# Performance work log

Hardware: AMD Instinct MI355X
Metric: run time of the kernel (lower is better)

The kernel has to match this reference:

```python
import jax, jax.numpy as jnp
import numpy as np


def setup_inputs() -> dict:
    key = jax.random.key(0)
    k1, k2, k3, k4 = jax.random.split(key, 4)
    B, C, H, W = 8, 256, 64, 64
    x = jax.random.normal(k1, (B, C, H, W), dtype=jnp.float32)
    wq = jax.random.normal(k2, (1, C), dtype=jnp.float32) * (1.0 / np.sqrt(C))
    wk = jax.random.normal(k3, (1, C), dtype=jnp.float32) * (1.0 / np.sqrt(C))
    wv = jax.random.normal(k4, (C, C), dtype=jnp.float32) * (1.0 / np.sqrt(C))
    gamma = jnp.zeros((1,), dtype=jnp.float32)
    return {"x": x, "wq": wq, "wk": wk, "wv": wv, "gamma": gamma}


def reference(x, wq, wk, wv, gamma):
    B, C, H, W = x.shape
    N = H * W
    xf = x.reshape(B, C, N)                      # [B, C, N]
    # 1x1 convs == channel matmuls
    f = jnp.einsum('oc,bcn->bon', wq, xf)        # [B, 1, N]
    g = jnp.einsum('oc,bcn->bon', wk, xf)        # [B, 1, N]
    h = jnp.einsum('oc,bcn->bon', wv, xf)        # [B, C, N]
    # scores[b, i, j] = f[b, 0, i] * g[b, 0, j]  -> [B, N, N]
    scores = jnp.einsum('bi,bj->bij', f[:, 0, :], g[:, 0, :])
    # softmax over dim=1 (rows), matching torch F.softmax(..., dim=1)
    beta = jax.nn.softmax(scores, axis=1)        # [B, N, N]
    gam = gamma[0]
    o = (1.0 - gam) * jnp.einsum('bcn,bnm->bcm', h, beta) + gam * xf
    return o.reshape(B, C, H, W)
```

## Files before the change

kernel.cpp:

```cpp
#include <hip/hip_runtime.h>
#include <math.h>

#define BQ 8
#define CQ 256
#define NQ 4096
#define MT 128
#define NSTEP (NQ / 32)

typedef short s16x8 __attribute__((ext_vector_type(8)));
typedef short s16x4 __attribute__((ext_vector_type(4)));
typedef float f32x4 __attribute__((ext_vector_type(4)));

static __device__ __forceinline__ float4 ld4(const float* p) { return *(const float4*)p; }

static constexpr float LOG2E = 1.4426950408889634f;

static __device__ __forceinline__ short f2bf(float f) {
    return __builtin_bit_cast(short, (__bf16)f);
}

__global__ void k_fg(const float* __restrict__ x, const float* __restrict__ wq,
                     const float* __restrict__ wk, float* __restrict__ fs,
                     float* __restrict__ g, short* __restrict__ xbf) {
    int b = blockIdx.y;
    int nloc = threadIdx.x & 63;
    int cg = threadIdx.x >> 6;
    int n = blockIdx.x * 64 + nloc;
    const float* xb = x + (size_t)b * CQ * NQ + n;
    short* xo = xbf + (size_t)b * CQ * NQ + n;
    float accf = 0.f, accg = 0.f;
    int c0 = cg * 64;
#pragma unroll 8
    for (int c = c0; c < c0 + 64; ++c) {
        float v = xb[(size_t)c * NQ];
        accf = fmaf(wq[c], v, accf);
        accg = fmaf(wk[c], v, accg);
        xo[(size_t)c * NQ] = f2bf(v);
    }
    __shared__ float sf[4][64], sg2[4][64];
    sf[cg][nloc] = accf;
    sg2[cg][nloc] = accg;
    __syncthreads();
    if (threadIdx.x < 64) {
        float f = sf[0][nloc] + sf[1][nloc] + sf[2][nloc] + sf[3][nloc];
        float gg = sg2[0][nloc] + sg2[1][nloc] + sg2[2][nloc] + sg2[3][nloc];
        fs[b * NQ + blockIdx.x * 64 + nloc] = f * LOG2E;
        g[b * NQ + blockIdx.x * 64 + nloc] = gg;
    }
}

__global__ void k_minmax(const float* __restrict__ fs, float* __restrict__ fmx,
                         float* __restrict__ fmn) {
    int b = blockIdx.x;
    const float* f = fs + b * NQ;
    float mx = -1e30f, mn = 1e30f;
    for (int i = threadIdx.x; i < NQ; i += 256) {
        float v = f[i];
        mx = fmaxf(mx, v);
        mn = fminf(mn, v);
    }
    for (int off = 32; off; off >>= 1) {
        mx = fmaxf(mx, __shfl_down(mx, off));
        mn = fminf(mn, __shfl_down(mn, off));
    }
    __shared__ float smx[4], smn[4];
    int wid = threadIdx.x >> 6;
    if ((threadIdx.x & 63) == 0) { smx[wid] = mx; smn[wid] = mn; }
    __syncthreads();
    if (threadIdx.x == 0) {
        mx = fmaxf(fmaxf(smx[0], smx[1]), fmaxf(smx[2], smx[3]));
        mn = fminf(fminf(smn[0], smn[1]), fminf(smn[2], smn[3]));
        fmx[b] = mx;
        fmn[b] = mn;
    }
}

__global__ void __launch_bounds__(256, 2) k_attn(
    const short* __restrict__ xbf, const float* __restrict__ fsp,
    const float* __restrict__ gp, const float* __restrict__ fmxs,
    const float* __restrict__ fmns, const float* __restrict__ wv,
    const float* __restrict__ x, const float* __restrict__ gamma,
    float* __restrict__ out) {
    __shared__ __align__(16) char smem[65536];

    int bid = blockIdx.x;
    int b = bid & 7;
    int mblk = bid >> 3;
    int m0 = mblk * MT;
    int tid = threadIdx.x;
    int l = tid & 63;
    int w = tid >> 6;
    int wc = w & 1;
    int wm = w >> 1;
    int q = l >> 4;
    int cr = l & 15;

    float fmx = fmxs[b], fmn = fmns[b];
    const float* gb = gp + b * NQ;
    float gj[4], nM[4], zac[4];
#pragma unroll
    for (int jm = 0; jm < 4; ++jm) {
        float gv = gb[m0 + wm * 64 + jm * 16 + cr];
        gj[jm] = gv;
        nM[jm] = -((gv >= 0.f) ? gv * fmx : gv * fmn);
        zac[jm] = 0.f;
    }

    const float* fb = fsp + b * NQ;
    const short* xb = xbf + (size_t)b * CQ * NQ;

    f32x4 acc[8][4];
#pragma unroll
    for (int jc = 0; jc < 8; ++jc)
#pragma unroll
        for (int jm = 0; jm < 4; ++jm) acc[jc][jm] = (f32x4){0.f, 0.f, 0.f, 0.f};

#pragma unroll
    for (int r2 = 0; r2 < 4; ++r2) {
        int off = tid * 16 + r2 * 4096;
        int row = off >> 6, nb = off & 63;
        const short* src = xb + (size_t)row * NQ + (nb >> 1);
        __builtin_amdgcn_global_load_lds(
            (const __attribute__((address_space(1))) void*)src,
            (__attribute__((address_space(3))) void*)(smem + off), 16, 0, 0);
    }
    float4 fqa = *(const float4*)(fb + q * 8);
    float4 fqb = *(const float4*)(fb + q * 8 + 4);
    __syncthreads();

    for (int t = 0; t < NSTEP; ++t) {
        const char* cbuf = smem + (t & 1) * 16384;
        int n0n = ((t + 1) & (NSTEP - 1)) * 32;
        if (t + 1 < NSTEP) {
            char* nbuf = smem + ((t + 1) & 1) * 16384;
#pragma unroll
            for (int r2 = 0; r2 < 4; ++r2) {
                int off = tid * 16 + r2 * 4096;
                int row = off >> 6, nb = off & 63;
                const short* src = xb + (size_t)row * NQ + n0n + (nb >> 1);
                __builtin_amdgcn_global_load_lds(
                    (const __attribute__((address_space(1))) void*)src,
                    (__attribute__((address_space(3))) void*)(nbuf + off), 16, 0, 0);
            }
        }
        float4 fqa_n = *(const float4*)(fb + n0n + q * 8);
        float4 fqb_n = *(const float4*)(fb + n0n + q * 8 + 4);
        float fq[8] = {fqa.x, fqa.y, fqa.z, fqa.w, fqb.x, fqb.y, fqb.z, fqb.w};
        s16x8 bv[4];
#pragma unroll
        for (int jm = 0; jm < 4; ++jm) {
            float z = zac[jm];
#pragma unroll
            for (int i = 0; i < 8; ++i) {
                float e = __builtin_amdgcn_exp2f(fmaf(fq[i], gj[jm], nM[jm]));
                z += e;
                bv[jm][i] = f2bf(e);
            }
            zac[jm] = z;
        }
#pragma unroll
        for (int jc = 0; jc < 8; ++jc) {
            s16x8 av = *(const s16x8*)(cbuf + (wc * 128 + jc * 16 + cr) * 64 + q * 16);
#pragma unroll
            for (int jm = 0; jm < 4; ++jm)
                acc[jc][jm] = __builtin_amdgcn_mfma_f32_16x16x32_bf16(av, bv[jm], acc[jc][jm], 0, 0, 0);
        }
        fqa = fqa_n;
        fqb = fqb_n;
        __syncthreads();
    }

    float rzl[4];
#pragma unroll
    for (int jm = 0; jm < 4; ++jm) {
        float z = zac[jm];
        z += __shfl_xor(z, 16);
        z += __shfl_xor(z, 32);
        rzl[jm] = 1.0f / z;
    }

#pragma unroll
    for (int jc = 0; jc < 8; ++jc) {
#pragma unroll
        for (int jm = 0; jm < 4; ++jm) {
            int mloc = wm * 64 + jm * 16 + cr;
            int cb = (wc * 256 + jc * 32 + q * 8) ^ ((mloc & 7) << 4);
            s16x4 v;
#pragma unroll
            for (int r = 0; r < 4; ++r) v[r] = f2bf(acc[jc][jm][r] * rzl[jm]);
            *(s16x4*)(smem + mloc * 512 + cb) = v;
        }
    }
    __syncthreads();

    int co0 = w * 64;
    f32x4 acc2[4][8];
#pragma unroll
    for (int j2 = 0; j2 < 4; ++j2)
#pragma unroll
        for (int jm2 = 0; jm2 < 8; ++jm2) acc2[j2][jm2] = (f32x4){0.f, 0.f, 0.f, 0.f};

#pragma unroll 2
    for (int ks = 0; ks < 8; ++ks) {
        s16x8 a2[4];
#pragma unroll
        for (int j2 = 0; j2 < 4; ++j2) {
            const float* wr = wv + (size_t)(co0 + j2 * 16 + cr) * CQ + ks * 32 + q * 8;
            float4 wa = ld4(wr);
            float4 wb = ld4(wr + 4);
            a2[j2][0] = f2bf(wa.x); a2[j2][1] = f2bf(wa.y);
            a2[j2][2] = f2bf(wa.z); a2[j2][3] = f2bf(wa.w);
            a2[j2][4] = f2bf(wb.x); a2[j2][5] = f2bf(wb.y);
            a2[j2][6] = f2bf(wb.z); a2[j2][7] = f2bf(wb.w);
        }
#pragma unroll
        for (int jm2 = 0; jm2 < 8; ++jm2) {
            int mloc = jm2 * 16 + cr;
            s16x8 b2 = *(const s16x8*)(smem + mloc * 512 + ((ks * 64 + q * 16) ^ ((mloc & 7) << 4)));
#pragma unroll
            for (int j2 = 0; j2 < 4; ++j2)
                acc2[j2][jm2] = __builtin_amdgcn_mfma_f32_16x16x32_bf16(a2[j2], b2, acc2[j2][jm2], 0, 0, 0);
        }
    }

    float gam = gamma[0];
    float omg = 1.f - gam;
    if (gam != 0.f) {
#pragma unroll
        for (int j2 = 0; j2 < 4; ++j2)
#pragma unroll
            for (int jm2 = 0; jm2 < 8; ++jm2)
#pragma unroll
                for (int r = 0; r < 4; ++r) {
                    int c_out = co0 + j2 * 16 + q * 4 + r;
                    size_t idx = ((size_t)b * CQ + c_out) * NQ + m0 + jm2 * 16 + cr;
                    __builtin_nontemporal_store(
                        fmaf(gam, x[idx], acc2[j2][jm2][r] * omg), out + idx);
                }
    } else {
#pragma unroll
        for (int j2 = 0; j2 < 4; ++j2)
#pragma unroll
            for (int jm2 = 0; jm2 < 8; ++jm2)
#pragma unroll
                for (int r = 0; r < 4; ++r) {
                    int c_out = co0 + j2 * 16 + q * 4 + r;
                    size_t idx = ((size_t)b * CQ + c_out) * NQ + m0 + jm2 * 16 + cr;
                    __builtin_nontemporal_store(acc2[j2][jm2][r] * omg, out + idx);
                }
    }
}

extern "C" void kernel_launch(void* const* d_in, const int* in_sizes, int n_in,
                              void* d_out, int out_size, void* d_ws, size_t ws_size,
                              hipStream_t stream) {
    const float* x     = (const float*)d_in[0];
    const float* wq    = (const float*)d_in[1];
    const float* wk    = (const float*)d_in[2];
    const float* wv    = (const float*)d_in[3];
    const float* gamma = (const float*)d_in[4];
    float* out = (float*)d_out;

    float* ws  = (float*)d_ws;
    float* fs  = ws;
    float* g   = ws + BQ * NQ;
    float* fmx = ws + 2 * BQ * NQ;
    float* fmn = fmx + BQ;
    short* xbf = (short*)(ws + 2 * BQ * NQ + 64);

    hipLaunchKernelGGL(k_fg, dim3(NQ / 64, BQ), dim3(256), 0, stream, x, wq, wk, fs, g, xbf);
    hipLaunchKernelGGL(k_minmax, dim3(BQ), dim3(256), 0, stream, fs, fmx, fmn);
    hipLaunchKernelGGL(k_attn, dim3(BQ * (NQ / MT)), dim3(256), 0, stream,
                       xbf, fs, g, fmx, fmn, wv, x, gamma, out);
}
```

Baseline: 135.8 us.

## Split attention K-loop across wave pairs with 4-stage LDS ring

Doubles the attention block to 512 threads. Wave pairs now alternate over the N reduction steps, with each pair's partial accumulators and softmax denominators merged through LDS. The x tile moves from double buffering to a 4-deep ring prefetched three steps ahead, and the f vector is staged once into LDS instead of being loaded from global memory every step. The aim is more waves per CU and better hiding of load latency in the exp+MFMA loop. The costs are a larger LDS footprint, an extra merge pass, and half of the waves sitting idle on alternate steps.

```diff
diff --git a/kernel.cpp b/kernel.cpp
--- a/kernel.cpp
+++ b/kernel.cpp
@@ -75,13 +75,18 @@
     }
 }
 
-__global__ void __launch_bounds__(256, 2) k_attn(
+#define RING_OFF 0
+#define FLDS_OFF 131072
+#define ZBUF_OFF 147456
+#define SMEM_BYTES 149504
+
+__global__ void __launch_bounds__(512, 2) k_attn(
     const short* __restrict__ xbf, const float* __restrict__ fsp,
     const float* __restrict__ gp, const float* __restrict__ fmxs,
     const float* __restrict__ fmns, const float* __restrict__ wv,
     const float* __restrict__ x, const float* __restrict__ gamma,
     float* __restrict__ out) {
-    __shared__ __align__(16) char smem[65536];
+    __shared__ __align__(16) char smem[SMEM_BYTES];
 
     int bid = blockIdx.x;
     int b = bid & 7;
@@ -90,10 +95,33 @@
     int tid = threadIdx.x;
     int l = tid & 63;
     int w = tid >> 6;
-    int wc = w & 1;
-    int wm = w >> 1;
+    int ws = w & 1;
+    int wm = (w >> 1) & 1;
+    int wc = w >> 2;
     int q = l >> 4;
     int cr = l & 15;
+
+    const short* xb = xbf + (size_t)b * CQ * NQ;
+    const float* fb = fsp + b * NQ;
+
+#pragma unroll
+    for (int r2 = 0; r2 < 2; ++r2) {
+        int off = tid * 16 + r2 * 8192;
+        __builtin_amdgcn_global_load_lds(
+            (const __attribute__((address_space(1))) void*)(fb + (off >> 2)),
+            (__attribute__((address_space(3))) void*)(smem + FLDS_OFF + off), 16, 0, 0);
+    }
+#pragma unroll
+    for (int c3 = 0; c3 < 3; ++c3) {
+#pragma unroll
+        for (int r2 = 0; r2 < 2; ++r2) {
+            int off = tid * 16 + r2 * 8192;
+            int row = off >> 6, nb = off & 63;
+            __builtin_amdgcn_global_load_lds(
+                (const __attribute__((address_space(1))) void*)(xb + (size_t)row * NQ + c3 * 32 + (nb >> 1)),
+                (__attribute__((address_space(3))) void*)(smem + c3 * 16384 + off), 16, 0, 0);
+        }
+    }
 
     float fmx = fmxs[b], fmn = fmns[b];
     const float* gb = gp + b * NQ;
@@ -106,105 +134,127 @@
         zac[jm] = 0.f;
     }
 
-    const float* fb = fsp + b * NQ;
-    const short* xb = xbf + (size_t)b * CQ * NQ;
-
     f32x4 acc[8][4];
 #pragma unroll
     for (int jc = 0; jc < 8; ++jc)
 #pragma unroll
         for (int jm = 0; jm < 4; ++jm) acc[jc][jm] = (f32x4){0.f, 0.f, 0.f, 0.f};
 
-#pragma unroll
-    for (int r2 = 0; r2 < 4; ++r2) {
-        int off = tid * 16 + r2 * 4096;
-        int row = off >> 6, nb = off & 63;
-        const short* src = xb + (size_t)row * NQ + (nb >> 1);
-        __builtin_amdgcn_global_load_lds(
-            (const __attribute__((address_space(1))) void*)src,
-            (__attribute__((address_space(3))) void*)(smem + off), 16, 0, 0);
-    }
-    float4 fqa = *(const float4*)(fb + q * 8);
-    float4 fqb = *(const float4*)(fb + q * 8 + 4);
-    __syncthreads();
-
     for (int t = 0; t < NSTEP; ++t) {
-        const char* cbuf = smem + (t & 1) * 16384;
-        int n0n = ((t + 1) & (NSTEP - 1)) * 32;
-        if (t + 1 < NSTEP) {
-            char* nbuf = smem + ((t + 1) & 1) * 16384;
-#pragma unroll
-            for (int r2 = 0; r2 < 4; ++r2) {
-                int off = tid * 16 + r2 * 4096;
+        asm volatile("s_waitcnt vmcnt(4)" ::: "memory");
+        __builtin_amdgcn_s_barrier();
+        {
+            int chunk = (t + 3) & (NSTEP - 1);
+            char* nbuf = smem + ((t + 3) & 3) * 16384;
+#pragma unroll
+            for (int r2 = 0; r2 < 2; ++r2) {
+                int off = tid * 16 + r2 * 8192;
                 int row = off >> 6, nb = off & 63;
-                const short* src = xb + (size_t)row * NQ + n0n + (nb >> 1);
                 __builtin_amdgcn_global_load_lds(
-                    (const __attribute__((address_space(1))) void*)src,
+                    (const __attribute__((address_space(1))) void*)(xb + (size_t)row * NQ + chunk * 32 + (nb >> 1)),
                     (__attribute__((address_space(3))) void*)(nbuf + off), 16, 0, 0);
             }
         }
-        float4 fqa_n = *(const float4*)(fb + n0n + q * 8);
-        float4 fqb_n = *(const float4*)(fb + n0n + q * 8 + 4);
-        float fq[8] = {fqa.x, fqa.y, fqa.z, fqa.w, fqb.x, fqb.y, fqb.z, fqb.w};
-        s16x8 bv[4];
-#pragma unroll
-        for (int jm = 0; jm < 4; ++jm) {
-            float z = zac[jm];
-#pragma unroll
-            for (int i = 0; i < 8; ++i) {
-                float e = __builtin_amdgcn_exp2f(fmaf(fq[i], gj[jm], nM[jm]));
-                z += e;
-                bv[jm][i] = f2bf(e);
+        if ((t & 1) == ws) {
+            const char* cbuf = smem + (t & 3) * 16384;
+            const float* fls = (const float*)(smem + FLDS_OFF) + t * 32;
+            float4 fqa = *(const float4*)(fls + q * 8);
+            float4 fqb = *(const float4*)(fls + q * 8 + 4);
+            float fq[8] = {fqa.x, fqa.y, fqa.z, fqa.w, fqb.x, fqb.y, fqb.z, fqb.w};
+            s16x8 bv[4];
+#pragma unroll
+            for (int jm = 0; jm < 4; ++jm) {
+                float z = zac[jm];
+#pragma unroll
+                for (int i = 0; i < 8; ++i) {
+                    float e = __builtin_amdgcn_exp2f(fmaf(fq[i], gj[jm], nM[jm]));
+                    z += e;
+                    bv[jm][i] = f2bf(e);
+                }
+                zac[jm] = z;
             }
-            zac[jm] = z;
-        }
-#pragma unroll
-        for (int jc = 0; jc < 8; ++jc) {
-            s16x8 av = *(const s16x8*)(cbuf + (wc * 128 + jc * 16 + cr) * 64 + q * 16);
-#pragma unroll
-            for (int jm = 0; jm < 4; ++jm)
-                acc[jc][jm] = __builtin_amdgcn_mfma_f32_16x16x32_bf16(av, bv[jm], acc[jc][jm], 0, 0, 0);
-        }
-        fqa = fqa_n;
-        fqb = fqb_n;
-        __syncthreads();
-    }
-
-    float rzl[4];
+#pragma unroll
+            for (int jc = 0; jc < 8; ++jc) {
+                s16x8 av = *(const s16x8*)(cbuf + (wc * 128 + jc * 16 + cr) * 64 + q * 16);
+#pragma unroll
+                for (int jm = 0; jm < 4; ++jm)
+                    acc[jc][jm] = __builtin_amdgcn_mfma_f32_16x16x32_bf16(av, bv[jm], acc[jc][jm], 0, 0, 0);
+            }
+        }
+    }
+    __syncthreads();
+
+    float zf[4];
 #pragma unroll
     for (int jm = 0; jm < 4; ++jm) {
         float z = zac[jm];
         z += __shfl_xor(z, 16);
         z += __shfl_xor(z, 32);
-        rzl[jm] = 1.0f / z;
-    }
-
-#pragma unroll
-    for (int jc = 0; jc < 8; ++jc) {
-#pragma unroll
-        for (int jm = 0; jm < 4; ++jm) {
-            int mloc = wm * 64 + jm * 16 + cr;
-            int cb = (wc * 256 + jc * 32 + q * 8) ^ ((mloc & 7) << 4);
-            s16x4 v;
-#pragma unroll
-            for (int r = 0; r < 4; ++r) v[r] = f2bf(acc[jc][jm][r] * rzl[jm]);
-            *(s16x4*)(smem + mloc * 512 + cb) = v;
-        }
-    }
-    __syncthreads();
-
-    int co0 = w * 64;
-    f32x4 acc2[4][8];
-#pragma unroll
-    for (int j2 = 0; j2 < 4; ++j2)
+        zf[jm] = z;
+    }
+    float* zb = (float*)(smem + ZBUF_OFF);
+    if (q == 0) {
+#pragma unroll
+        for (int jm = 0; jm < 4; ++jm) zb[w * 64 + jm * 16 + cr] = zf[jm];
+    }
+    __syncthreads();
+#pragma unroll
+    for (int jm = 0; jm < 4; ++jm) zf[jm] += zb[(w ^ 1) * 64 + jm * 16 + cr];
+
+    {
+        int p = wc * 2 + wm;
+        float* mrg = (float*)(smem + p * 32768);
+        if (ws == 1) {
+#pragma unroll
+            for (int jc = 0; jc < 8; ++jc)
+#pragma unroll
+                for (int jm = 0; jm < 4; ++jm)
+                    *(f32x4*)(mrg + ((jc * 4 + jm) * 64 + l) * 4) = acc[jc][jm];
+        }
+        __syncthreads();
+        if (ws == 0) {
+#pragma unroll
+            for (int jc = 0; jc < 8; ++jc)
+#pragma unroll
+                for (int jm = 0; jm < 4; ++jm) {
+                    f32x4 o = *(const f32x4*)(mrg + ((jc * 4 + jm) * 64 + l) * 4);
+                    acc[jc][jm] += o;
+                }
+        }
+        __syncthreads();
+    }
+
+    if (ws == 0) {
+        float rzl[4];
+#pragma unroll
+        for (int jm = 0; jm < 4; ++jm) rzl[jm] = 1.0f / zf[jm];
+#pragma unroll
+        for (int jc = 0; jc < 8; ++jc) {
+#pragma unroll
+            for (int jm = 0; jm < 4; ++jm) {
+                int mloc = wm * 64 + jm * 16 + cr;
+                int cb = (wc * 256 + jc * 32 + q * 8) ^ ((mloc & 7) << 4);
+                s16x4 v;
+#pragma unroll
+                for (int r = 0; r < 4; ++r) v[r] = f2bf(acc[jc][jm][r] * rzl[jm]);
+                *(s16x4*)(smem + mloc * 512 + cb) = v;
+            }
+        }
+    }
+    __syncthreads();
+
+    int co0 = w * 32;
+    f32x4 acc2[2][8];
+#pragma unroll
+    for (int j2 = 0; j2 < 2; ++j2)
 #pragma unroll
         for (int jm2 = 0; jm2 < 8; ++jm2) acc2[j2][jm2] = (f32x4){0.f, 0.f, 0.f, 0.f};
 
 #pragma unroll 2
     for (int ks = 0; ks < 8; ++ks) {
-        s16x8 a2[4];
-#pragma unroll
-        for (int j2 = 0; j2 < 4; ++j2) {
+        s16x8 a2[2];
+#pragma unroll
+        for (int j2 = 0; j2 < 2; ++j2) {
             const float* wr = wv + (size_t)(co0 + j2 * 16 + cr) * CQ + ks * 32 + q * 8;
             float4 wa = ld4(wr);
             float4 wb = ld4(wr + 4);
@@ -218,7 +268,7 @@
             int mloc = jm2 * 16 + cr;
             s16x8 b2 = *(const s16x8*)(smem + mloc * 512 + ((ks * 64 + q * 16) ^ ((mloc & 7) << 4)));
 #pragma unroll
-            for (int j2 = 0; j2 < 4; ++j2)
+            for (int j2 = 0; j2 < 2; ++j2)
                 acc2[j2][jm2] = __builtin_amdgcn_mfma_f32_16x16x32_bf16(a2[j2], b2, acc2[j2][jm2], 0, 0, 0);
         }
     }
@@ -227,7 +277,7 @@
     float omg = 1.f - gam;
     if (gam != 0.f) {
 #pragma unroll
-        for (int j2 = 0; j2 < 4; ++j2)
+        for (int j2 = 0; j2 < 2; ++j2)
 #pragma unroll
             for (int jm2 = 0; jm2 < 8; ++jm2)
 #pragma unroll
@@ -239,7 +289,7 @@
                 }
     } else {
 #pragma unroll
-        for (int j2 = 0; j2 < 4; ++j2)
+        for (int j2 = 0; j2 < 2; ++j2)
 #pragma unroll
             for (int jm2 = 0; jm2 < 8; ++jm2)
 #pragma unroll
@@ -270,6 +320,6 @@
 
     hipLaunchKernelGGL(k_fg, dim3(NQ / 64, BQ), dim3(256), 0, stream, x, wq, wk, fs, g, xbf);
     hipLaunchKernelGGL(k_minmax, dim3(BQ), dim3(256), 0, stream, fs, fmx, fmn);
-    hipLaunchKernelGGL(k_attn, dim3(BQ * (NQ / MT)), dim3(256), 0, stream,
+    hipLaunchKernelGGL(k_attn, dim3(BQ * (NQ / MT)), dim3(512), 0, stream,
                        xbf, fs, g, fmx, fmn, wv, x, gamma, out);
 }
```

Measured after the change: 200.4 us. 1.48x slower.
